# Performance work log

Measured on AMD Instinct MI355X. Metric: run time of the kernel, lower is better.

## Reference

```python
import jax, jax.numpy as jnp
import numpy as np

B, S, E = 4, 2048, 1024
H, D = 16, 64  # num_heads, head_dim_out; total_dim_out = H*D = 1024


def setup_inputs() -> dict:
    key = jax.random.key(0)
    ks = jax.random.split(key, 6)
    scale = 0.02
    X = jax.random.normal(ks[0], (B, S, E), dtype=jnp.float32)
    Wq = jax.random.normal(ks[1], (E, H * D), dtype=jnp.float32) * scale
    Wk = jax.random.normal(ks[2], (E, H * D), dtype=jnp.float32) * scale
    Wv = jax.random.normal(ks[3], (E, H * D), dtype=jnp.float32) * scale
    Wo = jax.random.normal(ks[4], (H * D, H * D), dtype=jnp.float32) * scale
    bo = jax.random.normal(ks[5], (H * D,), dtype=jnp.float32) * scale
    return {"X": X, "Wq": Wq, "Wk": Wk, "Wv": Wv, "Wo": Wo, "bo": bo}


def reference(X, Wq, Wk, Wv, Wo, bo):
    b, s, e = X.shape
    # projections -> [b, H, s, D]
    q = (X @ Wq).reshape(b, s, H, D).transpose(0, 2, 1, 3)
    k = (X @ Wk).reshape(b, s, H, D).transpose(0, 2, 1, 3)
    v = (X @ Wv).reshape(b, s, H, D).transpose(0, 2, 1, 3)
    # scores [b, H, s, s]; causal mask (strict upper triangle -> -inf) applied
    # before scaling, matching the original (sign of -inf is unchanged by scaling)
    scores = jnp.einsum("bhqd,bhkd->bhqk", q, k)
    causal = jnp.triu(jnp.ones((s, s), dtype=bool), k=1)
    scores = jnp.where(causal, -jnp.inf, scores)
    attn = jax.nn.softmax(scores / jnp.sqrt(jnp.float32(D)), axis=-1)
    # dropout_p = 0.0 -> identity
    ctx = jnp.einsum("bhqk,bhkd->bqhd", attn, v).reshape(b, s, H * D)
    return ctx @ Wo + bo
```

## Files before the change

kernel.cpp:

```cpp
#include <hip/hip_runtime.h>
#include <hip/hip_bf16.h>

typedef __bf16 bf16;
typedef __bf16 bf16x8 __attribute__((ext_vector_type(8)));
typedef float  f32x4  __attribute__((ext_vector_type(4)));
typedef unsigned short ushort_t;

#define Bsz 4
#define Ssz 2048
#define Esz 1024
#define Hn  16
#define Dh  64
#define HD  1024
#define QSCALE 0.1803368801111204f
#define M2 17.0f

#define SWZ(row, col) (((row) << 6) + ((((col) >> 3) ^ ((row) & 7)) << 3) + ((col) & 7))

__device__ __forceinline__ float bf16_bits_to_f32(ushort_t u) {
    union { unsigned int i; float f; } c;
    c.i = ((unsigned int)u) << 16;
    return c.f;
}

__global__ void detect_dtype(const ushort_t* __restrict__ Xbits, int* __restrict__ flag) {
    __shared__ float wmax[4];
    int tid = threadIdx.x, wave = tid >> 6, lane = tid & 63;
    size_t base = ((size_t)blockIdx.x * 256 + tid) * 8;
    ushort_t u[8];
    *(uint4*)u = *(const uint4*)&Xbits[base];
    float mx = 0.f;
    for (int i = 0; i < 8; i++)
        mx = fmaxf(mx, fabsf(bf16_bits_to_f32(u[i])));
    for (int off = 1; off < 64; off <<= 1)
        mx = fmaxf(mx, __shfl_xor(mx, off));
    if (lane == 0) wmax[wave] = mx;
    __syncthreads();
    if (tid == 0) {
        float m = fmaxf(fmaxf(wmax[0], wmax[1]), fmaxf(wmax[2], wmax[3]));
        flag[0] = (m > 1e6f) ? 1 : 0;
    }
}

__global__ void convert_x(const void* __restrict__ Xv, bf16* __restrict__ Xb,
                          const int* __restrict__ flag) {
    const int fl = flag[0];
    size_t off = ((size_t)blockIdx.x * 256 + threadIdx.x) * 8;
    if (fl) {
        const float* Xf = (const float*)Xv;
        float4 f0 = *(const float4*)&Xf[off];
        float4 f1 = *(const float4*)&Xf[off + 4];
        bf16 t[8] = {(bf16)f0.x, (bf16)f0.y, (bf16)f0.z, (bf16)f0.w,
                     (bf16)f1.x, (bf16)f1.y, (bf16)f1.z, (bf16)f1.w};
        *(uint4*)&Xb[off] = *(uint4*)t;
    } else {
        *(uint4*)&Xb[off] = *(const uint4*)&((const bf16*)Xv)[off];
    }
}

__global__ void transpose_w(const void* __restrict__ Wq, const void* __restrict__ Wk,
                            const void* __restrict__ Wv, const void* __restrict__ Wo,
                            bf16* TQ, bf16* TK, bf16* TV, bf16* TO,
                            const int* __restrict__ flag) {
    __shared__ bf16 t[64][68];
    const int fl = flag[0];
    const void* srcs[4] = {Wq, Wk, Wv, Wo};
    bf16*       dsts[4] = {TQ, TK, TV, TO};
    const void* src = srcs[blockIdx.z];
    bf16*       dst = dsts[blockIdx.z];
    int k0 = blockIdx.x * 64, n0 = blockIdx.y * 64;
    int tx = threadIdx.x, ty = threadIdx.y;
    for (int i = 0; i < 16; i++) {
        int r = i * 4 + ty;
        size_t idx = (size_t)(k0 + r) * 1024 + n0 + tx;
        float v = fl ? ((const float*)src)[idx] : (float)((const bf16*)src)[idx];
        t[r][tx] = (bf16)v;
    }
    __syncthreads();
    for (int i = 0; i < 16; i++) {
        int r = i * 4 + ty;
        dst[(size_t)(n0 + r) * 1024 + k0 + tx] = t[tx][r];
    }
}

__global__ __launch_bounds__(256, 2)
void gemm_qkv(const bf16* __restrict__ X,
              const bf16* __restrict__ WtQ, const bf16* __restrict__ WtK,
              const bf16* __restrict__ WtV,
              bf16* __restrict__ Qo, bf16* __restrict__ Ko, bf16* __restrict__ Vto) {
    const int mode = blockIdx.z;
    const bf16* Wt = (mode == 0) ? WtQ : (mode == 1) ? WtK : WtV;
    __shared__ __align__(16) bf16 smem[2 * 128 * 72];
    bf16 (*As)[72] = (bf16(*)[72])smem;
    bf16 (*Bs)[72] = (bf16(*)[72])(smem + 128 * 72);
    const int K = 1024;
    int tid = threadIdx.x;
    int wave = tid >> 6, lane = tid & 63;
    int qd = lane >> 4, c16 = lane & 15;
    int m0 = blockIdx.x * 128, n0 = blockIdx.y * 128;
    int wr = (wave >> 1) * 64, wc = (wave & 1) * 64;
    f32x4 acc[4][4] = {};

    for (int k0 = 0; k0 < K; k0 += 64) {
        for (int t = 0; t < 4; t++) {
            int c = tid + t * 256;
            int row = c >> 3, col = (c & 7) * 8;
            *(uint4*)&As[row][col] = *(const uint4*)&X [(size_t)(m0 + row) * K + k0 + col];
            *(uint4*)&Bs[row][col] = *(const uint4*)&Wt[(size_t)(n0 + row) * K + k0 + col];
        }
        __syncthreads();
        for (int kk = 0; kk < 64; kk += 32) {
            bf16x8 af[4], bfr[4];
            for (int mt = 0; mt < 4; mt++)
                af[mt] = *(const bf16x8*)&As[wr + mt * 16 + c16][kk + qd * 8];
            for (int nt = 0; nt < 4; nt++)
                bfr[nt] = *(const bf16x8*)&Bs[wc + nt * 16 + c16][kk + qd * 8];
            for (int mt = 0; mt < 4; mt++)
                for (int nt = 0; nt < 4; nt++)
                    acc[mt][nt] = __builtin_amdgcn_mfma_f32_16x16x32_bf16(
                        af[mt], bfr[nt], acc[mt][nt], 0, 0, 0);
        }
        __syncthreads();
    }

    if (mode == 2) {
        bf16 (*Tt)[136] = (bf16(*)[136])smem;
        for (int mt = 0; mt < 4; mt++)
            for (int nt = 0; nt < 4; nt++) {
                int nl = wc + nt * 16 + c16;
                int ml = wr + mt * 16 + qd * 4;
                bf16 q4[4] = {(bf16)acc[mt][nt][0], (bf16)acc[mt][nt][1],
                              (bf16)acc[mt][nt][2], (bf16)acc[mt][nt][3]};
                *(uint2*)&Tt[nl][ml] = *(uint2*)q4;
            }
        __syncthreads();
        int b = m0 >> 11, s0 = m0 & 2047;
        for (int i = 0; i < 8; i++) {
            int g = tid + i * 256;
            int row = g >> 4, col = (g & 15) * 8;
            int n = n0 + row;
            int h = n >> 6, d = n & 63;
            size_t idx = ((size_t)(b * Hn + h) * Dh + d) * Ssz + s0 + col;
            *(uint4*)&Vto[idx] = *(const uint4*)&Tt[row][col];
        }
    } else {
        const float qscale = (mode == 0) ? QSCALE : 1.0f;
        bf16* dst = (mode == 0) ? Qo : Ko;
        for (int mt = 0; mt < 4; mt++)
            for (int nt = 0; nt < 4; nt++)
                for (int r = 0; r < 4; r++) {
                    int m = m0 + wr + mt * 16 + qd * 4 + r;
                    int n = n0 + wc + nt * 16 + c16;
                    float v = acc[mt][nt][r] * qscale;
                    int b = m >> 11, s = m & 2047;
                    int h = n >> 6,  d = n & 63;
                    dst[((size_t)(b * Hn + h) * Ssz + s) * Dh + d] = (bf16)v;
                }
    }
}

__global__ __launch_bounds__(512, 4)
void attn(const bf16* __restrict__ Q, const bf16* __restrict__ K,
          const bf16* __restrict__ Vt, bf16* __restrict__ ctx) {
    int tid = threadIdx.x;
    int wave = tid >> 6, lane = tid & 63;
    int qd = lane >> 4, c16 = lane & 15;

    int bid = blockIdx.x;
    int xcd  = bid & 7;
    int slot = bid >> 3;
    int pr   = slot & 7;
    int bh   = xcd + ((slot >> 3) << 3);
    int b = bh >> 4, h = bh & 15;

    const bf16* Qp = Q  + (size_t)bh * Ssz * Dh;
    const bf16* Kp = K  + (size_t)bh * Ssz * Dh;
    const bf16* Vp = Vt + (size_t)bh * Dh * Ssz;

    __shared__ __align__(16) bf16 Ks_[64 * 64];
    __shared__ __align__(16) bf16 Vs_[64 * 64];
    __shared__ __align__(16) bf16 Pl[8][16][72];

    for (int half = 0; half < 2; half++) {
        int j = (half == 0) ? pr : (15 - pr);
        int q0 = j * 128 + wave * 16;

        bf16x8 qa0 = *(const bf16x8*)&Qp[(size_t)(q0 + c16) * Dh + qd * 8];
        bf16x8 qa1 = *(const bf16x8*)&Qp[(size_t)(q0 + c16) * Dh + 32 + qd * 8];

        f32x4 O[4] = {};
        float lsum[4] = {0.f, 0.f, 0.f, 0.f};

        int nkt = 2 * j + 2;
        for (int kt = 0; kt < nkt; kt++) {
            int kbase = kt * 64;
            __syncthreads();
            {
                int row = tid >> 3, col = (tid & 7) * 8;
                *(uint4*)&Ks_[SWZ(row, col)] = *(const uint4*)&Kp[(size_t)(kbase + row) * Dh + col];
                *(uint4*)&Vs_[SWZ(row, col)] = *(const uint4*)&Vp[(size_t)row * Ssz + kbase + col];
            }
            __syncthreads();

            if (kbase <= q0 + 15) {
                f32x4 sc[4] = {};
                for (int ct = 0; ct < 4; ct++) {
                    int row = ct * 16 + c16;
                    bf16x8 kf0 = *(const bf16x8*)&Ks_[SWZ(row, qd * 8)];
                    bf16x8 kf1 = *(const bf16x8*)&Ks_[SWZ(row, 32 + qd * 8)];
                    sc[ct] = __builtin_amdgcn_mfma_f32_16x16x32_bf16(qa0, kf0, sc[ct], 0, 0, 0);
                    sc[ct] = __builtin_amdgcn_mfma_f32_16x16x32_bf16(qa1, kf1, sc[ct], 0, 0, 0);
                }

                if (kbase + 63 > q0) {
                    for (int ct = 0; ct < 4; ct++)
                        for (int r = 0; r < 4; r++) {
                            int qrow = q0 + qd * 4 + r;
                            int key  = kbase + ct * 16 + c16;
                            float p = (key > qrow) ? 0.f : __builtin_exp2f(sc[ct][r] - M2);
                            sc[ct][r] = p;
                            lsum[r] += p;
                        }
                } else {
                    for (int ct = 0; ct < 4; ct++)
                        for (int r = 0; r < 4; r++) {
                            float p = __builtin_exp2f(sc[ct][r] - M2);
                            sc[ct][r] = p;
                            lsum[r] += p;
                        }
                }

                for (int ct = 0; ct < 4; ct++)
                    for (int r = 0; r < 4; r++)
                        Pl[wave][qd * 4 + r][ct * 16 + c16] = (bf16)sc[ct][r];
                asm volatile("s_waitcnt lgkmcnt(0)" ::: "memory");

                for (int kc = 0; kc < 2; kc++) {
                    bf16x8 pa = *(const bf16x8*)&Pl[wave][c16][kc * 32 + qd * 8];
                    for (int dt = 0; dt < 4; dt++) {
                        int row = dt * 16 + c16;
                        bf16x8 vb = *(const bf16x8*)&Vs_[SWZ(row, kc * 32 + qd * 8)];
                        O[dt] = __builtin_amdgcn_mfma_f32_16x16x32_bf16(pa, vb, O[dt], 0, 0, 0);
                    }
                }
            }
        }

        for (int off = 1; off < 16; off <<= 1)
            for (int r = 0; r < 4; r++)
                lsum[r] += __shfl_xor(lsum[r], off);
        float rinv[4];
        for (int r = 0; r < 4; r++) rinv[r] = 1.0f / lsum[r];

        for (int dt = 0; dt < 4; dt++)
            for (int r = 0; r < 4; r++) {
                int qrow = q0 + qd * 4 + r;
                int d = dt * 16 + c16;
                float v = O[dt][r] * rinv[r];
                ctx[(size_t)(b * Ssz + qrow) * HD + h * 64 + d] = (bf16)v;
            }
    }
}

__global__ __launch_bounds__(256, 2)
void gemm_out(const bf16* __restrict__ A, const bf16* __restrict__ WtO,
              const void* __restrict__ bo, void* __restrict__ outv,
              const int* __restrict__ flag) {
    __shared__ __align__(16) bf16 As[128][72];
    __shared__ __align__(16) bf16 Bs[128][72];
    const int fl = flag[0];
    const int K = 1024;
    int tid = threadIdx.x;
    int wave = tid >> 6, lane = tid & 63;
    int qd = lane >> 4, c16 = lane & 15;
    int m0 = blockIdx.x * 128, n0 = blockIdx.y * 128;
    int wr = (wave >> 1) * 64, wc = (wave & 1) * 64;
    f32x4 acc[4][4] = {};

    for (int k0 = 0; k0 < K; k0 += 64) {
        for (int t = 0; t < 4; t++) {
            int c = tid + t * 256;
            int row = c >> 3, col = (c & 7) * 8;
            *(uint4*)&As[row][col] = *(const uint4*)&A  [(size_t)(m0 + row) * K + k0 + col];
            *(uint4*)&Bs[row][col] = *(const uint4*)&WtO[(size_t)(n0 + row) * K + k0 + col];
        }
        __syncthreads();
        for (int kk = 0; kk < 64; kk += 32) {
            bf16x8 af[4], bfr[4];
            for (int mt = 0; mt < 4; mt++)
                af[mt] = *(const bf16x8*)&As[wr + mt * 16 + c16][kk + qd * 8];
            for (int nt = 0; nt < 4; nt++)
                bfr[nt] = *(const bf16x8*)&Bs[wc + nt * 16 + c16][kk + qd * 8];
            for (int mt = 0; mt < 4; mt++)
                for (int nt = 0; nt < 4; nt++)
                    acc[mt][nt] = __builtin_amdgcn_mfma_f32_16x16x32_bf16(
                        af[mt], bfr[nt], acc[mt][nt], 0, 0, 0);
        }
        __syncthreads();
    }

    for (int mt = 0; mt < 4; mt++)
        for (int nt = 0; nt < 4; nt++)
            for (int r = 0; r < 4; r++) {
                int m = m0 + wr + mt * 16 + qd * 4 + r;
                int n = n0 + wc + nt * 16 + c16;
                float bov = fl ? ((const float*)bo)[n] : (float)((const bf16*)bo)[n];
                float v = acc[mt][nt][r] + bov;
                size_t idx = (size_t)m * HD + n;
                if (fl) ((float*)outv)[idx] = v;
                else    ((bf16*)outv)[idx] = (bf16)v;
            }
}

extern "C" void kernel_launch(void* const* d_in, const int* in_sizes, int n_in,
                              void* d_out, int out_size, void* d_ws, size_t ws_size,
                              hipStream_t stream) {
    const void* X  = d_in[0];
    const void* Wq = d_in[1];
    const void* Wk = d_in[2];
    const void* Wv = d_in[3];
    const void* Wo = d_in[4];
    const void* bo = d_in[5];

    int*  flag = (int*)d_ws;
    bf16* ws   = (bf16*)d_ws + 64;
    const size_t WT = (size_t)1024 * 1024;
    const size_t QKV = (size_t)Bsz * Hn * Ssz * Dh;
    bf16* TQ  = ws;
    bf16* TK  = ws + WT;
    bf16* TV  = ws + 2 * WT;
    bf16* TO  = ws + 3 * WT;
    bf16* Qs  = ws + 4 * WT;
    bf16* Ks  = Qs + QKV;
    bf16* Vts = Ks + QKV;
    bf16* ctx = Vts + QKV;
    bf16* Xbf = ctx;

    detect_dtype<<<dim3(64), 256, 0, stream>>>((const ushort_t*)X, flag);
    convert_x<<<dim3(4096), 256, 0, stream>>>(X, Xbf, flag);
    transpose_w<<<dim3(16, 16, 4), dim3(64, 4), 0, stream>>>(Wq, Wk, Wv, Wo, TQ, TK, TV, TO, flag);
    gemm_qkv<<<dim3(64, 8, 3), 256, 0, stream>>>(Xbf, TQ, TK, TV, Qs, Ks, Vts);
    attn<<<dim3(512), 512, 0, stream>>>(Qs, Ks, Vts, ctx);
    gemm_out<<<dim3(64, 8), 256, 0, stream>>>(ctx, TO, bo, d_out, flag);
}
```

Before: 272.4 us.

## Use direct global-to-LDS loads in GEMMs and restructure attention tiling with register prefetch

Both projection GEMMs now fill shared memory with the global_load_lds intrinsic into XOR-swizzled tiles, replacing the padded layout and register staging. The attention kernel moves to 64-query blocks of 4 waves, doubling the grid, and prefetches the next K/V tile into registers while the current tile is computed. It also swaps the MFMA operand order so each lane owns one query row, which simplifies the row-sum reduction and allows vectorised P and output stores. This trades larger register use and new swizzle bookkeeping for less load latency and better causal work balance.

```diff
diff --git a/kernel.cpp b/kernel.cpp
--- a/kernel.cpp
+++ b/kernel.cpp
@@ -21,6 +21,12 @@
     union { unsigned int i; float f; } c;
     c.i = ((unsigned int)u) << 16;
     return c.f;
+}
+
+__device__ __forceinline__ void gload_lds16(const bf16* g, bf16* l) {
+    __builtin_amdgcn_global_load_lds(
+        (const __attribute__((address_space(1))) void*)g,
+        (__attribute__((address_space(3))) void*)l, 16, 0, 0);
 }
 
 __global__ void detect_dtype(const ushort_t* __restrict__ Xbits, int* __restrict__ flag) {
@@ -90,9 +96,9 @@
               bf16* __restrict__ Qo, bf16* __restrict__ Ko, bf16* __restrict__ Vto) {
     const int mode = blockIdx.z;
     const bf16* Wt = (mode == 0) ? WtQ : (mode == 1) ? WtK : WtV;
-    __shared__ __align__(16) bf16 smem[2 * 128 * 72];
-    bf16 (*As)[72] = (bf16(*)[72])smem;
-    bf16 (*Bs)[72] = (bf16(*)[72])(smem + 128 * 72);
+    __shared__ __align__(16) bf16 smem[17408];
+    bf16* As = smem;
+    bf16* Bs = smem + 8192;
     const int K = 1024;
     int tid = threadIdx.x;
     int wave = tid >> 6, lane = tid & 63;
@@ -103,18 +109,26 @@
 
     for (int k0 = 0; k0 < K; k0 += 64) {
         for (int t = 0; t < 4; t++) {
-            int c = tid + t * 256;
-            int row = c >> 3, col = (c & 7) * 8;
-            *(uint4*)&As[row][col] = *(const uint4*)&X [(size_t)(m0 + row) * K + k0 + col];
-            *(uint4*)&Bs[row][col] = *(const uint4*)&Wt[(size_t)(n0 + row) * K + k0 + col];
+            int g = t * 256 + tid;
+            int row = g >> 3, cgL = g & 7;
+            int cc = cgL ^ (row & 7);
+            bf16* lb = As + (t * 256 + wave * 64) * 8;
+            gload_lds16(&X[(size_t)(m0 + row) * K + k0 + cc * 8], lb);
+        }
+        for (int t = 0; t < 4; t++) {
+            int g = t * 256 + tid;
+            int row = g >> 3, cgL = g & 7;
+            int cc = cgL ^ (row & 7);
+            bf16* lb = Bs + (t * 256 + wave * 64) * 8;
+            gload_lds16(&Wt[(size_t)(n0 + row) * K + k0 + cc * 8], lb);
         }
         __syncthreads();
         for (int kk = 0; kk < 64; kk += 32) {
             bf16x8 af[4], bfr[4];
             for (int mt = 0; mt < 4; mt++)
-                af[mt] = *(const bf16x8*)&As[wr + mt * 16 + c16][kk + qd * 8];
+                af[mt] = *(const bf16x8*)&As[SWZ(wr + mt * 16 + c16, kk + qd * 8)];
             for (int nt = 0; nt < 4; nt++)
-                bfr[nt] = *(const bf16x8*)&Bs[wc + nt * 16 + c16][kk + qd * 8];
+                bfr[nt] = *(const bf16x8*)&Bs[SWZ(wc + nt * 16 + c16, kk + qd * 8)];
             for (int mt = 0; mt < 4; mt++)
                 for (int nt = 0; nt < 4; nt++)
                     acc[mt][nt] = __builtin_amdgcn_mfma_f32_16x16x32_bf16(
@@ -159,7 +173,7 @@
     }
 }
 
-__global__ __launch_bounds__(512, 4)
+__global__ __launch_bounds__(256, 4)
 void attn(const bf16* __restrict__ Q, const bf16* __restrict__ K,
           const bf16* __restrict__ Vt, bf16* __restrict__ ctx) {
     int tid = threadIdx.x;
@@ -169,8 +183,8 @@
     int bid = blockIdx.x;
     int xcd  = bid & 7;
     int slot = bid >> 3;
-    int pr   = slot & 7;
-    int bh   = xcd + ((slot >> 3) << 3);
+    int pr   = slot & 15;
+    int bh   = xcd + ((slot >> 4) << 3);
     int b = bh >> 4, h = bh & 15;
 
     const bf16* Qp = Q  + (size_t)bh * Ssz * Dh;
@@ -179,86 +193,96 @@
 
     __shared__ __align__(16) bf16 Ks_[64 * 64];
     __shared__ __align__(16) bf16 Vs_[64 * 64];
-    __shared__ __align__(16) bf16 Pl[8][16][72];
+    __shared__ __align__(16) bf16 Pl[4][16][80];
+
+    int srow = tid >> 3, scol = (tid & 7) * 8;
 
     for (int half = 0; half < 2; half++) {
-        int j = (half == 0) ? pr : (15 - pr);
-        int q0 = j * 128 + wave * 16;
+        int qb = (half == 0) ? pr : (31 - pr);
+        int q0 = qb * 64 + wave * 16;
+        int qrow = q0 + c16;
 
         bf16x8 qa0 = *(const bf16x8*)&Qp[(size_t)(q0 + c16) * Dh + qd * 8];
         bf16x8 qa1 = *(const bf16x8*)&Qp[(size_t)(q0 + c16) * Dh + 32 + qd * 8];
 
         f32x4 O[4] = {};
-        float lsum[4] = {0.f, 0.f, 0.f, 0.f};
-
-        int nkt = 2 * j + 2;
+        float lsum = 0.f;
+
+        int nkt = qb + 1;
+        uint4 kr0 = *(const uint4*)&Kp[(size_t)srow * Dh + scol];
+        uint4 kr1 = *(const uint4*)&Kp[(size_t)(srow + 32) * Dh + scol];
+        uint4 vr0 = *(const uint4*)&Vp[(size_t)srow * Ssz + scol];
+        uint4 vr1 = *(const uint4*)&Vp[(size_t)(srow + 32) * Ssz + scol];
+
         for (int kt = 0; kt < nkt; kt++) {
             int kbase = kt * 64;
             __syncthreads();
-            {
-                int row = tid >> 3, col = (tid & 7) * 8;
-                *(uint4*)&Ks_[SWZ(row, col)] = *(const uint4*)&Kp[(size_t)(kbase + row) * Dh + col];
-                *(uint4*)&Vs_[SWZ(row, col)] = *(const uint4*)&Vp[(size_t)row * Ssz + kbase + col];
-            }
+            *(uint4*)&Ks_[SWZ(srow,      scol)] = kr0;
+            *(uint4*)&Ks_[SWZ(srow + 32, scol)] = kr1;
+            *(uint4*)&Vs_[SWZ(srow,      scol)] = vr0;
+            *(uint4*)&Vs_[SWZ(srow + 32, scol)] = vr1;
             __syncthreads();
-
-            if (kbase <= q0 + 15) {
-                f32x4 sc[4] = {};
-                for (int ct = 0; ct < 4; ct++) {
-                    int row = ct * 16 + c16;
-                    bf16x8 kf0 = *(const bf16x8*)&Ks_[SWZ(row, qd * 8)];
-                    bf16x8 kf1 = *(const bf16x8*)&Ks_[SWZ(row, 32 + qd * 8)];
-                    sc[ct] = __builtin_amdgcn_mfma_f32_16x16x32_bf16(qa0, kf0, sc[ct], 0, 0, 0);
-                    sc[ct] = __builtin_amdgcn_mfma_f32_16x16x32_bf16(qa1, kf1, sc[ct], 0, 0, 0);
+            if (kt + 1 < nkt) {
+                int nb = kbase + 64;
+                kr0 = *(const uint4*)&Kp[(size_t)(nb + srow) * Dh + scol];
+                kr1 = *(const uint4*)&Kp[(size_t)(nb + srow + 32) * Dh + scol];
+                vr0 = *(const uint4*)&Vp[(size_t)srow * Ssz + nb + scol];
+                vr1 = *(const uint4*)&Vp[(size_t)(srow + 32) * Ssz + nb + scol];
+            }
+
+            f32x4 sc[4] = {};
+            for (int ct = 0; ct < 4; ct++) {
+                int row = ct * 16 + c16;
+                bf16x8 kf0 = *(const bf16x8*)&Ks_[SWZ(row, qd * 8)];
+                bf16x8 kf1 = *(const bf16x8*)&Ks_[SWZ(row, 32 + qd * 8)];
+                sc[ct] = __builtin_amdgcn_mfma_f32_16x16x32_bf16(kf0, qa0, sc[ct], 0, 0, 0);
+                sc[ct] = __builtin_amdgcn_mfma_f32_16x16x32_bf16(kf1, qa1, sc[ct], 0, 0, 0);
+            }
+
+            if (kt == qb) {
+                for (int ct = 0; ct < 4; ct++)
+                    for (int r = 0; r < 4; r++) {
+                        int key = kbase + ct * 16 + qd * 4 + r;
+                        float p = (key > qrow) ? 0.f : __builtin_exp2f(sc[ct][r] - M2);
+                        sc[ct][r] = p;
+                        lsum += p;
+                    }
+            } else {
+                for (int ct = 0; ct < 4; ct++)
+                    for (int r = 0; r < 4; r++) {
+                        float p = __builtin_exp2f(sc[ct][r] - M2);
+                        sc[ct][r] = p;
+                        lsum += p;
+                    }
+            }
+
+            for (int ct = 0; ct < 4; ct++) {
+                bf16 t4[4] = {(bf16)sc[ct][0], (bf16)sc[ct][1],
+                              (bf16)sc[ct][2], (bf16)sc[ct][3]};
+                *(uint2*)&Pl[wave][c16][ct * 16 + qd * 4] = *(uint2*)t4;
+            }
+            asm volatile("s_waitcnt lgkmcnt(0)" ::: "memory");
+
+            for (int kc = 0; kc < 2; kc++) {
+                bf16x8 pa = *(const bf16x8*)&Pl[wave][c16][kc * 32 + qd * 8];
+                for (int dt = 0; dt < 4; dt++) {
+                    int row = dt * 16 + c16;
+                    bf16x8 vb = *(const bf16x8*)&Vs_[SWZ(row, kc * 32 + qd * 8)];
+                    O[dt] = __builtin_amdgcn_mfma_f32_16x16x32_bf16(vb, pa, O[dt], 0, 0, 0);
                 }
-
-                if (kbase + 63 > q0) {
-                    for (int ct = 0; ct < 4; ct++)
-                        for (int r = 0; r < 4; r++) {
-                            int qrow = q0 + qd * 4 + r;
-                            int key  = kbase + ct * 16 + c16;
-                            float p = (key > qrow) ? 0.f : __builtin_exp2f(sc[ct][r] - M2);
-                            sc[ct][r] = p;
-                            lsum[r] += p;
-                        }
-                } else {
-                    for (int ct = 0; ct < 4; ct++)
-                        for (int r = 0; r < 4; r++) {
-                            float p = __builtin_exp2f(sc[ct][r] - M2);
-                            sc[ct][r] = p;
-                            lsum[r] += p;
-                        }
-                }
-
-                for (int ct = 0; ct < 4; ct++)
-                    for (int r = 0; r < 4; r++)
-                        Pl[wave][qd * 4 + r][ct * 16 + c16] = (bf16)sc[ct][r];
-                asm volatile("s_waitcnt lgkmcnt(0)" ::: "memory");
-
-                for (int kc = 0; kc < 2; kc++) {
-                    bf16x8 pa = *(const bf16x8*)&Pl[wave][c16][kc * 32 + qd * 8];
-                    for (int dt = 0; dt < 4; dt++) {
-                        int row = dt * 16 + c16;
-                        bf16x8 vb = *(const bf16x8*)&Vs_[SWZ(row, kc * 32 + qd * 8)];
-                        O[dt] = __builtin_amdgcn_mfma_f32_16x16x32_bf16(pa, vb, O[dt], 0, 0, 0);
-                    }
-                }
-            }
-        }
-
-        for (int off = 1; off < 16; off <<= 1)
-            for (int r = 0; r < 4; r++)
-                lsum[r] += __shfl_xor(lsum[r], off);
-        float rinv[4];
-        for (int r = 0; r < 4; r++) rinv[r] = 1.0f / lsum[r];
-
-        for (int dt = 0; dt < 4; dt++)
-            for (int r = 0; r < 4; r++) {
-                int qrow = q0 + qd * 4 + r;
-                int d = dt * 16 + c16;
-                float v = O[dt][r] * rinv[r];
-                ctx[(size_t)(b * Ssz + qrow) * HD + h * 64 + d] = (bf16)v;
-            }
+            }
+        }
+
+        lsum += __shfl_xor(lsum, 16);
+        lsum += __shfl_xor(lsum, 32);
+        float rinv = 1.0f / lsum;
+
+        for (int dt = 0; dt < 4; dt++) {
+            bf16 o4[4];
+            for (int r = 0; r < 4; r++) o4[r] = (bf16)(O[dt][r] * rinv);
+            *(uint2*)&ctx[(size_t)(b * Ssz + qrow) * HD + h * 64 + dt * 16 + qd * 4] =
+                *(uint2*)o4;
+        }
     }
 }
 
@@ -266,8 +290,9 @@
 void gemm_out(const bf16* __restrict__ A, const bf16* __restrict__ WtO,
               const void* __restrict__ bo, void* __restrict__ outv,
               const int* __restrict__ flag) {
-    __shared__ __align__(16) bf16 As[128][72];
-    __shared__ __align__(16) bf16 Bs[128][72];
+    __shared__ __align__(16) bf16 smem[16384];
+    bf16* As = smem;
+    bf16* Bs = smem + 8192;
     const int fl = flag[0];
     const int K = 1024;
     int tid = threadIdx.x;
@@ -279,18 +304,26 @@
 
     for (int k0 = 0; k0 < K; k0 += 64) {
         for (int t = 0; t < 4; t++) {
-            int c = tid + t * 256;
-            int row = c >> 3, col = (c & 7) * 8;
-            *(uint4*)&As[row][col] = *(const uint4*)&A  [(size_t)(m0 + row) * K + k0 + col];
-            *(uint4*)&Bs[row][col] = *(const uint4*)&WtO[(size_t)(n0 + row) * K + k0 + col];
+            int g = t * 256 + tid;
+            int row = g >> 3, cgL = g & 7;
+            int cc = cgL ^ (row & 7);
+            bf16* lb = As + (t * 256 + wave * 64) * 8;
+            gload_lds16(&A[(size_t)(m0 + row) * K + k0 + cc * 8], lb);
+        }
+        for (int t = 0; t < 4; t++) {
+            int g = t * 256 + tid;
+            int row = g >> 3, cgL = g & 7;
+            int cc = cgL ^ (row & 7);
+            bf16* lb = Bs + (t * 256 + wave * 64) * 8;
+            gload_lds16(&WtO[(size_t)(n0 + row) * K + k0 + cc * 8], lb);
         }
         __syncthreads();
         for (int kk = 0; kk < 64; kk += 32) {
             bf16x8 af[4], bfr[4];
             for (int mt = 0; mt < 4; mt++)
-                af[mt] = *(const bf16x8*)&As[wr + mt * 16 + c16][kk + qd * 8];
+                af[mt] = *(const bf16x8*)&As[SWZ(wr + mt * 16 + c16, kk + qd * 8)];
             for (int nt = 0; nt < 4; nt++)
-                bfr[nt] = *(const bf16x8*)&Bs[wc + nt * 16 + c16][kk + qd * 8];
+                bfr[nt] = *(const bf16x8*)&Bs[SWZ(wc + nt * 16 + c16, kk + qd * 8)];
             for (int mt = 0; mt < 4; mt++)
                 for (int nt = 0; nt < 4; nt++)
                     acc[mt][nt] = __builtin_amdgcn_mfma_f32_16x16x32_bf16(
@@ -340,6 +373,6 @@
     convert_x<<<dim3(4096), 256, 0, stream>>>(X, Xbf, flag);
     transpose_w<<<dim3(16, 16, 4), dim3(64, 4), 0, stream>>>(Wq, Wk, Wv, Wo, TQ, TK, TV, TO, flag);
     gemm_qkv<<<dim3(64, 8, 3), 256, 0, stream>>>(Xbf, TQ, TK, TV, Qs, Ks, Vts);
-    attn<<<dim3(512), 512, 0, stream>>>(Qs, Ks, Vts, ctx);
+    attn<<<dim3(1024), 256, 0, stream>>>(Qs, Ks, Vts, ctx);
     gemm_out<<<dim3(64, 8), 256, 0, stream>>>(ctx, TO, bo, d_out, flag);
 }
```

Result: no change. 267.2 us (-1.9%).
